# Kernel optimization log

Measured on AMD Instinct MI355X. Metric: run time of the kernel, lower is better.

## Reference

```python
import jax, jax.numpy as jnp
import numpy as np

NB_TS = 4          # module-level global nb_timestep in the original code
EMBED = 512
SQRT_DIM = float(np.sqrt(EMBED))


def _conv(x, w, b=None):
    # torch Conv2d(kernel=3, stride=1, padding=1), NCHW / OIHW
    y = jax.lax.conv_general_dilated(x, w, (1, 1), ((1, 1), (1, 1)),
                                     dimension_numbers=('NCHW', 'OIHW', 'NCHW'))
    if b is not None:
        y = y + b[None, :, None, None]
    return y


def setup_inputs() -> dict:
    B, C, H, W = 8, 512, 16, 16
    TXT = 256
    key = jax.random.key(0)
    ks = iter(jax.random.split(key, 40))

    def nrm(shape, s=0.02):
        return jax.random.normal(next(ks), shape, jnp.float32) * s

    inp = {
        'x':   jax.random.normal(next(ks), (B, C, H, W), jnp.float32),
        'txt': jax.random.normal(next(ks), (B, 1, TXT), jnp.float32),
        # attention convs
        'Wa_w': nrm((C, C, 3, 3)), 'Wa_b': nrm((C,)),
        'Ua_w': nrm((C, C, 3, 3)), 'Ua_b': nrm((C,)),
        'Va_w': nrm((1, C, 3, 3)),
        # gate convs
        'Wi_w': nrm((C, C, 3, 3)), 'Wi_b': nrm((C,)),
        'Ui_w': nrm((C, C, 3, 3)), 'Ui_b': nrm((C,)),
        'Wf_w': nrm((C, C, 3, 3)), 'Wf_b': nrm((C,)),
        'Uf_w': nrm((C, C, 3, 3)), 'Uf_b': nrm((C,)),
        'Wc_w': nrm((C, C, 3, 3)), 'Wc_b': nrm((C,)),
        'Uc_w': nrm((C, C, 3, 3)), 'Uc_b': nrm((C,)),
        'Wo_w': nrm((C, C, 3, 3)), 'Wo_b': nrm((C,)),
        'Uo_w': nrm((C, C, 3, 3)), 'Uo_b': nrm((C,)),
        # text attention linears (torch Linear weight layout [out, in])
        'WQ': nrm((EMBED * H * W, TXT)),
        'WK': nrm((EMBED, 1)),
        'WV': nrm((EMBED, 1)),
        'Wsum_w': nrm((1, EMBED)), 'Wsum_b': nrm((1,)),
    }
    return inp


def reference(x, txt, Wa_w, Wa_b, Ua_w, Ua_b, Va_w,
              Wi_w, Wi_b, Ui_w, Ui_b, Wf_w, Wf_b, Uf_w, Uf_b,
              Wc_w, Wc_b, Uc_w, Uc_b, Wo_w, Wo_b, Uo_w, Uo_b,
              WQ, WK, WV, Wsum_w, Wsum_b):
    B, _, Hs, Ws = x.shape
    txt2 = txt.reshape(txt.shape[0], txt.shape[2])  # [B, 256]
    h = x
    c = x
    # Q is timestep-invariant; hoist out of the loop (same math)
    Q = (txt2 @ WQ.T).reshape(B, Hs, Ws, EMBED)  # [B,H,W,E]
    for _ in range(NB_TS):
        Z = _conv(jnp.tanh(_conv(h, Wa_w, Wa_b) + _conv(x, Ua_w, Ua_b)), Va_w)  # [B,1,H,W]
        A1 = jax.nn.softmax(Z, axis=1)          # softmax over channel dim of size 1 (faithful)
        Ap = jnp.transpose(A1, (0, 2, 3, 1))    # [B,H,W,1]
        K = Ap @ WK.T                            # [B,H,W,E]
        V = Ap @ WV.T                            # [B,H,W,E]
        scores = jnp.sum(Q * K, axis=3, keepdims=True) / SQRT_DIM  # [B,H,W,1]
        attn = jax.nn.softmax(scores, axis=1)    # torch softmax(dim=1) -> over H axis
        # repeat(...,embed_dim)*V is just a broadcast multiply
        A2 = (attn * V) @ Wsum_w.T + Wsum_b      # [B,H,W,1]
        A2 = jnp.transpose(A2, (0, 3, 1, 2))     # [B,1,H,W]
        myA = A1 + A2
        AM = myA * x
        i = jax.nn.sigmoid(_conv(AM, Wi_w, Wi_b) + _conv(h, Ui_w, Ui_b))
        f = jax.nn.sigmoid(_conv(AM, Wf_w, Wf_b) + _conv(h, Uf_w, Uf_b))
        o = jax.nn.sigmoid(_conv(AM, Wo_w, Wo_b) + _conv(h, Uo_w, Uo_b))
        g = jnp.tanh(_conv(AM, Wc_w, Wc_b) + _conv(h, Uc_w, Uc_b))
        c = g * i + f * c
        h = jnp.tanh(c) * o
    return h
```

## Files before the change

### kernel.cpp

```cpp
#include <hip/hip_runtime.h>

typedef unsigned short u16;
typedef __attribute__((ext_vector_type(8))) _Float16 f16x8;
typedef __attribute__((ext_vector_type(4))) float f32x4;
typedef __attribute__((ext_vector_type(4))) int i32x4;
typedef __attribute__((ext_vector_type(4))) unsigned short us4;

__device__ __forceinline__ u16 f2h(float f) {
  _Float16 h = (_Float16)f;
  return __builtin_bit_cast(unsigned short, h);
}
__device__ __forceinline__ float sigm(float v) { return 1.0f / (1.0f + __expf(-v)); }
__device__ __forceinline__ float tanh_(float v) {
  float t = __expf(-2.0f * fabsf(v));
  float r = (1.0f - t) / (1.0f + t);
  return v >= 0.0f ? r : -r;
}

typedef const __attribute__((address_space(1))) unsigned int* gas_t;
typedef __attribute__((address_space(3))) unsigned int* las_t;
__device__ __forceinline__ void gl16(const u16* g, u16* l) {
  __builtin_amdgcn_global_load_lds((gas_t)g, (las_t)l, 16, 0, 0);
}

__global__ __launch_bounds__(256, 4) void prep_scores(
    const float* __restrict__ WQ, const float* __restrict__ WK,
    const float* __restrict__ txt, const float* __restrict__ WV,
    const float* __restrict__ Wsw, const float* __restrict__ Wsb,
    float* __restrict__ scores, float* __restrict__ sb) {
  __shared__ float red[4][8];
  __shared__ float red2[4];
  int tid = threadIdx.x;
  int p = blockIdx.x & 255;
  int es = blockIdx.x >> 8;
  int t4 = tid & 63, eg = tid >> 6;
  const f32x4* base = (const f32x4*)WQ + ((size_t)p * 512 + es * 64 + eg * 16) * 64 + t4;
  f32x4 va[16];
#pragma unroll
  for (int i = 0; i < 16; ++i) va[i] = base[i * 64];
  f32x4 wkq[4];
  const f32x4* wkp = (const f32x4*)(WK + es * 64 + eg * 16);
#pragma unroll
  for (int i = 0; i < 4; ++i) wkq[i] = wkp[i];
  __builtin_amdgcn_sched_barrier(0);
  f32x4 m4 = {0.f, 0.f, 0.f, 0.f};
#pragma unroll
  for (int i = 0; i < 4; ++i)
#pragma unroll
    for (int e = 0; e < 4; ++e) m4 += va[i * 4 + e] * wkq[i][e];
  float v[8];
  const f32x4* txp = (const f32x4*)txt;
#pragma unroll
  for (int b = 0; b < 8; ++b) {
    f32x4 tx = txp[b * 64 + t4];
    v[b] = m4[0] * tx[0] + m4[1] * tx[1] + m4[2] * tx[2] + m4[3] * tx[3];
  }
#pragma unroll
  for (int off = 32; off; off >>= 1)
#pragma unroll
    for (int b = 0; b < 8; ++b) v[b] += __shfl_down(v[b], off, 64);
  if (t4 == 0)
#pragma unroll
    for (int b = 0; b < 8; ++b) red[eg][b] = v[b];
  __syncthreads();
  if (tid < 8) {
    float sv = red[0][tid] + red[1][tid] + red[2][tid] + red[3][tid];
    atomicAdd(&scores[tid * 256 + p], sv * 0.044194173824159216f);
  }
  if (blockIdx.x == 0) {
    float vv = WV[tid] * Wsw[tid] + WV[tid + 256] * Wsw[tid + 256];
#pragma unroll
    for (int off = 32; off; off >>= 1) vv += __shfl_down(vv, off, 64);
    if (t4 == 0) red2[eg] = vv;
    __syncthreads();
    if (tid == 0) {
      sb[0] = red2[0] + red2[1] + red2[2] + red2[3];
      sb[1] = Wsb[0];
    }
  }
}

__global__ __launch_bounds__(256, 4) void prep_swz(
    const float* __restrict__ wi, const float* __restrict__ wf,
    const float* __restrict__ wo, const float* __restrict__ wc,
    const float* __restrict__ ui, const float* __restrict__ uf,
    const float* __restrict__ uo, const float* __restrict__ uc,
    u16* __restrict__ dstW, u16* __restrict__ dstU) {
  int tid = threadIdx.x;
  int sbid = blockIdx.x;
  int set = sbid >> 9;
  int chgrp = (sbid >> 4) & 31;
  int chunk = sbid & 15;
  int q = tid & 3, gch = tid >> 2;
  int gate = gch >> 4, chrow = gch & 15;
  int ch = chgrp * 16 + chrow;
  const float* s;
  if (set == 0) s = gate == 0 ? wi : gate == 1 ? wf : gate == 2 ? wo : wc;
  else          s = gate == 0 ? ui : gate == 1 ? uf : gate == 2 ? uo : uc;
  const f32x4* src = (const f32x4*)(s + (size_t)(ch * 512 + chunk * 32) * 9) + q * 18;
  f32x4 va[18];
#pragma unroll
  for (int i = 0; i < 18; ++i) va[i] = src[i];
  __builtin_amdgcn_sched_barrier(0);
  u16* dst = (set == 0 ? dstW : dstU) + (size_t)(chgrp * 16 + chunk) * 18432
             + (size_t)(gate * 64 + q * 16 + chrow) * 8;
#pragma unroll
  for (int k9 = 0; k9 < 9; ++k9) {
    i32x4 wv;
#pragma unroll
    for (int w = 0; w < 4; ++w) {
      int i0 = (2 * w) * 9 + k9, i1 = (2 * w + 1) * 9 + k9;
      unsigned lo = f2h(va[i0 >> 2][i0 & 3]);
      unsigned hi = f2h(va[i1 >> 2][i1 & 3]);
      wv[w] = (int)(lo | (hi << 16));
    }
    *(i32x4*)(dst + k9 * 2048) = wv;
  }
}

__global__ void prep_inputs(const float* __restrict__ x, const float* __restrict__ scores,
                            const float* __restrict__ sb,
                            u16* __restrict__ AM, u16* __restrict__ H0) {
  __shared__ float sc[16];
  int idx = blockIdx.x * 256 + threadIdx.x;
  int ch = idx & 511, p = (idx >> 9) & 255, b = idx >> 17;
  int w = p & 15, h = p >> 4;
  if (threadIdx.x < 16) sc[threadIdx.x] = scores[b * 256 + threadIdx.x * 16 + w];
  __syncthreads();
  float s = sb[0], b0 = sb[1];
  float mx = -1e30f;
#pragma unroll
  for (int hh = 0; hh < 16; ++hh) mx = fmaxf(mx, sc[hh]);
  float den = 0.f, my = 0.f;
#pragma unroll
  for (int hh = 0; hh < 16; ++hh) {
    float e = __expf(sc[hh] - mx);
    den += e;
    if (hh == h) my = e;
  }
  float coef = 1.0f + b0 + s * my / den;
  float xv = x[(size_t)(b * 512 + ch) * 256 + p];
  AM[idx] = f2h(coef * xv);
  H0[idx] = f2h(xv);
}

template <int MODE>
__launch_bounds__(512, 2)
__global__ void conv4(const u16* __restrict__ inA, const u16* __restrict__ inH,
                      const u16* __restrict__ wW, const u16* __restrict__ wU,
                      const float* __restrict__ bWi, const float* __restrict__ bUi,
                      const float* __restrict__ bWf, const float* __restrict__ bUf,
                      const float* __restrict__ bWo, const float* __restrict__ bUo,
                      const float* __restrict__ bWc, const float* __restrict__ bUc,
                      float* __restrict__ G, const float* __restrict__ c_src,
                      float* __restrict__ c_dst, u16* __restrict__ h_out,
                      float* __restrict__ out) {
  __shared__ __align__(16) u16 Alds[2][9 * 4 * 64 * 8];
  __shared__ __align__(16) u16 Blds[2][18 * 18 * 32];
  const int tid = threadIdx.x;
  const int chgrp = blockIdx.x & 31;
  const int b = blockIdx.x >> 5;
  const int wave = tid >> 6, lane = tid & 63;
  const int row = lane & 15, quad = lane >> 4;
  const int nw = wave & 3, mw = wave >> 2;
  const int NCH = (MODE == 0) ? 32 : 16;

  {
    i32x4 z = {0, 0, 0, 0};
    i32x4* bz = (i32x4*)&Blds[0][0];
#pragma unroll
    for (int i = 0; i < 6; ++i) {
      int k = tid + 512 * i;
      if (k < 2592) bz[k] = z;
    }
  }
  __syncthreads();

  const u16* wsrcW = wW + (size_t)chgrp * 294912;
  const u16* wsrcU = wU + (size_t)chgrp * 294912;
  const u16* isrcA = inA + (size_t)b * 131072;
  const u16* isrcH = inH + (size_t)b * 131072;

  auto stage = [&](int k, int bb) {
    const u16* gw;
    const u16* gi;
    if (MODE == 0 && k < 16) { gw = wsrcW + k * 18432; gi = isrcA + k * 32; }
    else                     { gw = wsrcU + (k & 15) * 18432; gi = isrcH + (k & 15) * 32; }
    u16* Ab = &Alds[bb][0];
#pragma unroll
    for (int i = 0; i < 5; ++i) {
      int idx = i * 8 + wave;
      if (idx < 36) gl16(gw + (idx * 64 + lane) * 8, &Ab[idx * 512]);
    }
    u16* Bb = &Blds[bb][0];
    int xi = lane >> 2;
    int qsrc = (lane & 3) ^ (((xi + 1) >> 2) & 3);
#pragma unroll
    for (int j = 0; j < 2; ++j) {
      int gy = wave + j * 8;
      gl16(gi + (size_t)(gy * 16 + xi) * 512 + qsrc * 8, &Bb[(gy + 1) * 576 + 32]);
    }
  };

  f32x4 acc[2][4];
#pragma unroll
  for (int m = 0; m < 2; ++m)
#pragma unroll
    for (int jj = 0; jj < 4; ++jj) acc[m][jj] = (f32x4){0.f, 0.f, 0.f, 0.f};

  const int ch0 = chgrp * 16 + quad * 4;
  float* gptr = G + (size_t)blockIdx.x * 16384 + wave * 2048 + lane * 4;

  stage(0, 0);
  __syncthreads();
  int bb = 0;

#pragma unroll 1
  for (int k = 0; k < NCH; ++k) {
    if (k + 1 < NCH) stage(k + 1, bb ^ 1);
    const u16* Ab = &Alds[bb][0];
    const u16* Bb = &Blds[bb][0];
#pragma unroll
    for (int kx = 0; kx < 3; ++kx) {
      int xx = row + kx;
      int qs = quad ^ ((xx >> 2) & 3);
      f16x8 bfr[6];
#pragma unroll
      for (int rr = 0; rr < 6; ++rr)
        bfr[rr] = *(const f16x8*)(&Bb[(4 * nw + rr) * 576 + xx * 32 + qs * 8]);
      f16x8 afr[6];
#pragma unroll
      for (int ky = 0; ky < 3; ++ky)
#pragma unroll
        for (int m = 0; m < 2; ++m)
          afr[ky * 2 + m] = *(const f16x8*)(&Ab[((ky * 3 + kx) * 4 + 2 * mw + m) * 512 + lane * 8]);
#pragma unroll
      for (int ky = 0; ky < 3; ++ky)
#pragma unroll
        for (int m = 0; m < 2; ++m)
#pragma unroll
          for (int jj = 0; jj < 4; ++jj)
            acc[m][jj] = __builtin_amdgcn_mfma_f32_16x16x32_f16(afr[ky * 2 + m], bfr[jj + ky],
                                                                acc[m][jj], 0, 0, 0);
    }
    if constexpr (MODE == 0) {
      if (k == 15) {
#pragma unroll
        for (int m = 0; m < 2; ++m) {
          int g = 2 * mw + m;
          const float* bw = g == 0 ? bWi : g == 1 ? bWf : g == 2 ? bWo : bWc;
          const float* bu = g == 0 ? bUi : g == 1 ? bUf : g == 2 ? bUo : bUc;
          f32x4 bias;
#pragma unroll
          for (int r = 0; r < 4; ++r) bias[r] = bw[ch0 + r] + bu[ch0 + r];
#pragma unroll
          for (int jj = 0; jj < 4; ++jj) {
            acc[m][jj] = acc[m][jj] + bias;
            *(f32x4*)(gptr + (m * 4 + jj) * 256) = acc[m][jj];
          }
        }
      }
    }
    __syncthreads();
    bb ^= 1;
  }

  if constexpr (MODE != 0) {
#pragma unroll
    for (int m = 0; m < 2; ++m)
#pragma unroll
      for (int jj = 0; jj < 4; ++jj)
        acc[m][jj] = acc[m][jj] + *(const f32x4*)(gptr + (m * 4 + jj) * 256);
  }
  float* X = (float*)&Blds[0][0];
  if (mw == 1) {
#pragma unroll
    for (int m = 0; m < 2; ++m)
#pragma unroll
      for (int jj = 0; jj < 4; ++jj)
        *(f32x4*)(X + (size_t)(((nw * 2 + m) * 4 + jj) * 256) + lane * 4) = acc[m][jj];
  }
  __syncthreads();
  if (mw == 0) {
#pragma unroll
    for (int jj = 0; jj < 4; ++jj) {
      const int p = (4 * nw + jj) * 16 + row;
      f32x4 zi = acc[0][jj], zf = acc[1][jj];
      f32x4 zo = *(const f32x4*)(X + (size_t)(((nw * 2 + 0) * 4 + jj) * 256) + lane * 4);
      f32x4 zg = *(const f32x4*)(X + (size_t)(((nw * 2 + 1) * 4 + jj) * 256) + lane * 4);
      f32x4 cold;
#pragma unroll
      for (int r = 0; r < 4; ++r)
        cold[r] = c_src[(size_t)(b * 512 + ch0 + r) * 256 + p];
      f32x4 cnew, hv;
#pragma unroll
      for (int r = 0; r < 4; ++r) {
        float iv = sigm(zi[r]);
        float fv = sigm(zf[r]);
        float ov = sigm(zo[r]);
        float gv = tanh_(zg[r]);
        float cn = fmaf(gv, iv, fv * cold[r]);
        cnew[r] = cn;
        hv[r] = tanh_(cn) * ov;
      }
      if constexpr (MODE != 2) {
#pragma unroll
        for (int r = 0; r < 4; ++r)
          c_dst[(size_t)(b * 512 + ch0 + r) * 256 + p] = cnew[r];
        us4 hb;
        hb[0] = f2h(hv[0]); hb[1] = f2h(hv[1]);
        hb[2] = f2h(hv[2]); hb[3] = f2h(hv[3]);
        *(us4*)(h_out + (size_t)b * 131072 + (size_t)p * 512 + ch0) = hb;
      } else {
#pragma unroll
        for (int r = 0; r < 4; ++r)
          out[(size_t)(b * 512 + ch0 + r) * 256 + p] = hv[r];
      }
    }
  }
}

extern "C" void kernel_launch(void* const* d_in, const int* in_sizes, int n_in,
                              void* d_out, int out_size, void* d_ws, size_t ws_size,
                              hipStream_t stream) {
  const float* x    = (const float*)d_in[0];
  const float* txt  = (const float*)d_in[1];
  const float* Wi_w = (const float*)d_in[7];
  const float* Wi_b = (const float*)d_in[8];
  const float* Ui_w = (const float*)d_in[9];
  const float* Ui_b = (const float*)d_in[10];
  const float* Wf_w = (const float*)d_in[11];
  const float* Wf_b = (const float*)d_in[12];
  const float* Uf_w = (const float*)d_in[13];
  const float* Uf_b = (const float*)d_in[14];
  const float* Wc_w = (const float*)d_in[15];
  const float* Wc_b = (const float*)d_in[16];
  const float* Uc_w = (const float*)d_in[17];
  const float* Uc_b = (const float*)d_in[18];
  const float* Wo_w = (const float*)d_in[19];
  const float* Wo_b = (const float*)d_in[20];
  const float* Uo_w = (const float*)d_in[21];
  const float* Uo_b = (const float*)d_in[22];
  const float* WQ   = (const float*)d_in[23];
  const float* WK   = (const float*)d_in[24];
  const float* WV   = (const float*)d_in[25];
  const float* Wsw  = (const float*)d_in[26];
  const float* Wsb  = (const float*)d_in[27];
  (void)in_sizes; (void)n_in; (void)ws_size;

  char* ws = (char*)d_ws;
  size_t off = 0;
  auto carve = [&](size_t n) {
    char* p = ws + off;
    off += (n + 255) & ~(size_t)255;
    return p;
  };
  u16* WswzW    = (u16*)carve(18874368);
  u16* WswzU    = (u16*)carve(18874368);
  u16* AM       = (u16*)carve(2097152);
  u16* H0       = (u16*)carve(2097152);
  u16* H1       = (u16*)carve(2097152);
  float* G      = (float*)carve(16777216);
  float* C      = (float*)carve(4194304);
  float* scores = (float*)carve(8192);
  float* sb     = (float*)carve(256);

  hipMemsetAsync(scores, 0, 8192, stream);

  prep_scores<<<2048, 256, 0, stream>>>(WQ, WK, txt, WV, Wsw, Wsb, scores, sb);
  prep_swz<<<1024, 256, 0, stream>>>(Wi_w, Wf_w, Wo_w, Wc_w,
                                     Ui_w, Uf_w, Uo_w, Uc_w, WswzW, WswzU);
  prep_inputs<<<4096, 256, 0, stream>>>(x, scores, sb, AM, H0);

  conv4<0><<<256, 512, 0, stream>>>(AM, H0, WswzW, WswzU,
                                    Wi_b, Ui_b, Wf_b, Uf_b, Wo_b, Uo_b, Wc_b, Uc_b,
                                    G, x, C, H1, nullptr);
  conv4<1><<<256, 512, 0, stream>>>(nullptr, H1, nullptr, WswzU,
                                    nullptr, nullptr, nullptr, nullptr,
                                    nullptr, nullptr, nullptr, nullptr,
                                    G, C, C, H0, nullptr);
  conv4<1><<<256, 512, 0, stream>>>(nullptr, H0, nullptr, WswzU,
                                    nullptr, nullptr, nullptr, nullptr,
                                    nullptr, nullptr, nullptr, nullptr,
                                    G, C, C, H1, nullptr);
  conv4<2><<<256, 512, 0, stream>>>(nullptr, H1, nullptr, WswzU,
                                    nullptr, nullptr, nullptr, nullptr,
                                    nullptr, nullptr, nullptr, nullptr,
                                    G, C, nullptr, nullptr, (float*)d_out);
}
```

Baseline: 508.2 us.

## Store activations pre-padded, split conv blocks by row half, restage prep loads

Activations AM/H0/H1 are now stored in a zero-padded 18x18 NHWC layout, so the conv kernel reads input fragments straight from global memory instead of staging the image tile through LDS. Each batch image is split across two blocks by row half, which doubles the grid and raises the occupancy target. The WQ score kernel now loads through LDS with global_load_lds, and the weight swizzle kernel uses 512 threads with smaller per-thread chunks. The cost is extra memsets for the padded buffers, and the conv B-operand reads now go uncached through global/L2 with redundant loads across waves, trading LDS traffic for more latency and memory traffic.

```diff
diff --git a/kernel.cpp b/kernel.cpp
--- a/kernel.cpp
+++ b/kernel.cpp
@@ -23,45 +23,45 @@
   __builtin_amdgcn_global_load_lds((gas_t)g, (las_t)l, 16, 0, 0);
 }
 
-__global__ __launch_bounds__(256, 4) void prep_scores(
+__global__ __launch_bounds__(256) void prep_scores(
     const float* __restrict__ WQ, const float* __restrict__ WK,
     const float* __restrict__ txt, const float* __restrict__ WV,
     const float* __restrict__ Wsw, const float* __restrict__ Wsb,
     float* __restrict__ scores, float* __restrict__ sb) {
+  __shared__ __align__(16) float L[64 * 256];
+  __shared__ float wk[64];
   __shared__ float red[4][8];
   __shared__ float red2[4];
   int tid = threadIdx.x;
+  int lane = tid & 63, wave = tid >> 6;
   int p = blockIdx.x & 255;
   int es = blockIdx.x >> 8;
-  int t4 = tid & 63, eg = tid >> 6;
-  const f32x4* base = (const f32x4*)WQ + ((size_t)p * 512 + es * 64 + eg * 16) * 64 + t4;
-  f32x4 va[16];
-#pragma unroll
-  for (int i = 0; i < 16; ++i) va[i] = base[i * 64];
-  f32x4 wkq[4];
-  const f32x4* wkp = (const f32x4*)(WK + es * 64 + eg * 16);
-#pragma unroll
-  for (int i = 0; i < 4; ++i) wkq[i] = wkp[i];
-  __builtin_amdgcn_sched_barrier(0);
-  f32x4 m4 = {0.f, 0.f, 0.f, 0.f};
-#pragma unroll
-  for (int i = 0; i < 4; ++i)
-#pragma unroll
-    for (int e = 0; e < 4; ++e) m4 += va[i * 4 + e] * wkq[i][e];
+  const float* src = WQ + ((size_t)p * 512 + es * 64 + wave * 16) * 256;
+  u16* ldst = (u16*)&L[wave * 16 * 256];
+#pragma unroll
+  for (int r = 0; r < 16; ++r)
+    gl16((const u16*)(src + (size_t)r * 256 + lane * 4), ldst + r * 512);
+  if (tid < 64) wk[tid] = WK[es * 64 + tid];
+  __syncthreads();
+  float a0 = 0.f, a1 = 0.f, a2 = 0.f, a3 = 0.f;
+#pragma unroll
+  for (int e = 0; e < 64; e += 4) {
+    a0 = fmaf(L[(e + 0) * 256 + tid], wk[e + 0], a0);
+    a1 = fmaf(L[(e + 1) * 256 + tid], wk[e + 1], a1);
+    a2 = fmaf(L[(e + 2) * 256 + tid], wk[e + 2], a2);
+    a3 = fmaf(L[(e + 3) * 256 + tid], wk[e + 3], a3);
+  }
+  float m = (a0 + a1) + (a2 + a3);
   float v[8];
-  const f32x4* txp = (const f32x4*)txt;
-#pragma unroll
-  for (int b = 0; b < 8; ++b) {
-    f32x4 tx = txp[b * 64 + t4];
-    v[b] = m4[0] * tx[0] + m4[1] * tx[1] + m4[2] * tx[2] + m4[3] * tx[3];
-  }
+#pragma unroll
+  for (int b = 0; b < 8; ++b) v[b] = m * txt[b * 256 + tid];
 #pragma unroll
   for (int off = 32; off; off >>= 1)
 #pragma unroll
     for (int b = 0; b < 8; ++b) v[b] += __shfl_down(v[b], off, 64);
-  if (t4 == 0)
-#pragma unroll
-    for (int b = 0; b < 8; ++b) red[eg][b] = v[b];
+  if (lane == 0)
+#pragma unroll
+    for (int b = 0; b < 8; ++b) red[wave][b] = v[b];
   __syncthreads();
   if (tid < 8) {
     float sv = red[0][tid] + red[1][tid] + red[2][tid] + red[3][tid];
@@ -71,7 +71,7 @@
     float vv = WV[tid] * Wsw[tid] + WV[tid + 256] * Wsw[tid + 256];
 #pragma unroll
     for (int off = 32; off; off >>= 1) vv += __shfl_down(vv, off, 64);
-    if (t4 == 0) red2[eg] = vv;
+    if (lane == 0) red2[wave] = vv;
     __syncthreads();
     if (tid == 0) {
       sb[0] = red2[0] + red2[1] + red2[2] + red2[3];
@@ -80,41 +80,37 @@
   }
 }
 
-__global__ __launch_bounds__(256, 4) void prep_swz(
+__global__ __launch_bounds__(512) void prep_swz(
     const float* __restrict__ wi, const float* __restrict__ wf,
     const float* __restrict__ wo, const float* __restrict__ wc,
     const float* __restrict__ ui, const float* __restrict__ uf,
     const float* __restrict__ uo, const float* __restrict__ uc,
     u16* __restrict__ dstW, u16* __restrict__ dstU) {
   int tid = threadIdx.x;
-  int sbid = blockIdx.x;
-  int set = sbid >> 9;
-  int chgrp = (sbid >> 4) & 31;
-  int chunk = sbid & 15;
-  int q = tid & 3, gch = tid >> 2;
-  int gate = gch >> 4, chrow = gch & 15;
+  int set = blockIdx.x >> 9;
+  int chgrp = (blockIdx.x >> 4) & 31;
+  int chunk = blockIdx.x & 15;
+  int gate = tid >> 7, chrow = (tid >> 3) & 15, oct = tid & 7;
+  int q = oct >> 1, c0 = (oct & 1) * 4;
   int ch = chgrp * 16 + chrow;
   const float* s;
   if (set == 0) s = gate == 0 ? wi : gate == 1 ? wf : gate == 2 ? wo : wc;
   else          s = gate == 0 ? ui : gate == 1 ? uf : gate == 2 ? uo : uc;
-  const f32x4* src = (const f32x4*)(s + (size_t)(ch * 512 + chunk * 32) * 9) + q * 18;
-  f32x4 va[18];
-#pragma unroll
-  for (int i = 0; i < 18; ++i) va[i] = src[i];
-  __builtin_amdgcn_sched_barrier(0);
+  const f32x4* src = (const f32x4*)(s + ((size_t)(ch * 512 + chunk * 32) + q * 8 + c0) * 9);
+  f32x4 va[9];
+#pragma unroll
+  for (int i = 0; i < 9; ++i) va[i] = src[i];
   u16* dst = (set == 0 ? dstW : dstU) + (size_t)(chgrp * 16 + chunk) * 18432
-             + (size_t)(gate * 64 + q * 16 + chrow) * 8;
+             + (size_t)(gate * 64 + q * 16 + chrow) * 8 + c0;
 #pragma unroll
   for (int k9 = 0; k9 < 9; ++k9) {
-    i32x4 wv;
-#pragma unroll
-    for (int w = 0; w < 4; ++w) {
-      int i0 = (2 * w) * 9 + k9, i1 = (2 * w + 1) * 9 + k9;
-      unsigned lo = f2h(va[i0 >> 2][i0 & 3]);
-      unsigned hi = f2h(va[i1 >> 2][i1 & 3]);
-      wv[w] = (int)(lo | (hi << 16));
-    }
-    *(i32x4*)(dst + k9 * 2048) = wv;
+    us4 wv;
+#pragma unroll
+    for (int c = 0; c < 4; ++c) {
+      int i = c * 9 + k9;
+      wv[c] = f2h(va[i >> 2][i & 3]);
+    }
+    *(us4*)(dst + (size_t)k9 * 2048) = wv;
   }
 }
 
@@ -140,12 +136,13 @@
   }
   float coef = 1.0f + b0 + s * my / den;
   float xv = x[(size_t)(b * 512 + ch) * 256 + p];
-  AM[idx] = f2h(coef * xv);
-  H0[idx] = f2h(xv);
+  size_t o = (size_t)b * 165888 + (size_t)((h + 1) * 18 + (w + 1)) * 512 + ch;
+  AM[o] = f2h(coef * xv);
+  H0[o] = f2h(xv);
 }
 
 template <int MODE>
-__launch_bounds__(512, 2)
+__launch_bounds__(512, 4)
 __global__ void conv4(const u16* __restrict__ inA, const u16* __restrict__ inH,
                       const u16* __restrict__ wW, const u16* __restrict__ wU,
                       const float* __restrict__ bWi, const float* __restrict__ bUi,
@@ -156,93 +153,74 @@
                       float* __restrict__ c_dst, u16* __restrict__ h_out,
                       float* __restrict__ out) {
   __shared__ __align__(16) u16 Alds[2][9 * 4 * 64 * 8];
-  __shared__ __align__(16) u16 Blds[2][18 * 18 * 32];
   const int tid = threadIdx.x;
   const int chgrp = blockIdx.x & 31;
-  const int b = blockIdx.x >> 5;
+  const int nhalf = (blockIdx.x >> 5) & 1;
+  const int b = blockIdx.x >> 6;
   const int wave = tid >> 6, lane = tid & 63;
   const int row = lane & 15, quad = lane >> 4;
   const int nw = wave & 3, mw = wave >> 2;
   const int NCH = (MODE == 0) ? 32 : 16;
-
-  {
-    i32x4 z = {0, 0, 0, 0};
-    i32x4* bz = (i32x4*)&Blds[0][0];
-#pragma unroll
-    for (int i = 0; i < 6; ++i) {
-      int k = tid + 512 * i;
-      if (k < 2592) bz[k] = z;
-    }
-  }
-  __syncthreads();
+  const int r0 = nhalf * 8 + nw * 2;
 
   const u16* wsrcW = wW + (size_t)chgrp * 294912;
   const u16* wsrcU = wU + (size_t)chgrp * 294912;
-  const u16* isrcA = inA + (size_t)b * 131072;
-  const u16* isrcH = inH + (size_t)b * 131072;
-
-  auto stage = [&](int k, int bb) {
-    const u16* gw;
-    const u16* gi;
-    if (MODE == 0 && k < 16) { gw = wsrcW + k * 18432; gi = isrcA + k * 32; }
-    else                     { gw = wsrcU + (k & 15) * 18432; gi = isrcH + (k & 15) * 32; }
+  const u16* imgA = inA + (size_t)b * 165888;
+  const u16* imgH = inH + (size_t)b * 165888;
+
+  auto stageA = [&](int k, int bb) {
+    const u16* gw = (MODE == 0 && k < 16) ? wsrcW + k * 18432 : wsrcU + (k & 15) * 18432;
     u16* Ab = &Alds[bb][0];
 #pragma unroll
     for (int i = 0; i < 5; ++i) {
       int idx = i * 8 + wave;
       if (idx < 36) gl16(gw + (idx * 64 + lane) * 8, &Ab[idx * 512]);
     }
-    u16* Bb = &Blds[bb][0];
-    int xi = lane >> 2;
-    int qsrc = (lane & 3) ^ (((xi + 1) >> 2) & 3);
-#pragma unroll
-    for (int j = 0; j < 2; ++j) {
-      int gy = wave + j * 8;
-      gl16(gi + (size_t)(gy * 16 + xi) * 512 + qsrc * 8, &Bb[(gy + 1) * 576 + 32]);
-    }
   };
 
-  f32x4 acc[2][4];
+  f32x4 acc[2][2];
 #pragma unroll
   for (int m = 0; m < 2; ++m)
 #pragma unroll
-    for (int jj = 0; jj < 4; ++jj) acc[m][jj] = (f32x4){0.f, 0.f, 0.f, 0.f};
+    for (int n = 0; n < 2; ++n) acc[m][n] = (f32x4){0.f, 0.f, 0.f, 0.f};
 
   const int ch0 = chgrp * 16 + quad * 4;
-  float* gptr = G + (size_t)blockIdx.x * 16384 + wave * 2048 + lane * 4;
-
-  stage(0, 0);
+  float* gptr = G + (size_t)blockIdx.x * 8192 + wave * 1024 + lane * 4;
+
+  stageA(0, 0);
   __syncthreads();
   int bb = 0;
 
 #pragma unroll 1
   for (int k = 0; k < NCH; ++k) {
-    if (k + 1 < NCH) stage(k + 1, bb ^ 1);
+    if (k + 1 < NCH) stageA(k + 1, bb ^ 1);
+    const u16* img = (MODE == 0 && k < 16) ? imgA : imgH;
+    const u16* ibase = img + (size_t)(k & 15) * 32 + quad * 8;
+    f16x8 bfr[3][4];
+#pragma unroll
+    for (int kx = 0; kx < 3; ++kx)
+#pragma unroll
+      for (int jj = 0; jj < 4; ++jj)
+        bfr[kx][jj] = *(const f16x8*)(ibase + (size_t)((r0 + jj) * 18 + row + kx) * 512);
     const u16* Ab = &Alds[bb][0];
-    const u16* Bb = &Blds[bb][0];
 #pragma unroll
     for (int kx = 0; kx < 3; ++kx) {
-      int xx = row + kx;
-      int qs = quad ^ ((xx >> 2) & 3);
-      f16x8 bfr[6];
-#pragma unroll
-      for (int rr = 0; rr < 6; ++rr)
-        bfr[rr] = *(const f16x8*)(&Bb[(4 * nw + rr) * 576 + xx * 32 + qs * 8]);
       f16x8 afr[6];
 #pragma unroll
       for (int ky = 0; ky < 3; ++ky)
 #pragma unroll
         for (int m = 0; m < 2; ++m)
-          afr[ky * 2 + m] = *(const f16x8*)(&Ab[((ky * 3 + kx) * 4 + 2 * mw + m) * 512 + lane * 8]);
+          afr[ky * 2 + m] = *(const f16x8*)(&Alds[bb][((ky * 3 + kx) * 4 + 2 * mw + m) * 512 + lane * 8]);
 #pragma unroll
       for (int ky = 0; ky < 3; ++ky)
 #pragma unroll
         for (int m = 0; m < 2; ++m)
 #pragma unroll
-          for (int jj = 0; jj < 4; ++jj)
-            acc[m][jj] = __builtin_amdgcn_mfma_f32_16x16x32_f16(afr[ky * 2 + m], bfr[jj + ky],
-                                                                acc[m][jj], 0, 0, 0);
-    }
+          for (int n = 0; n < 2; ++n)
+            acc[m][n] = __builtin_amdgcn_mfma_f32_16x16x32_f16(afr[ky * 2 + m], bfr[kx][n + ky],
+                                                               acc[m][n], 0, 0, 0);
+    }
+    (void)Ab;
     if constexpr (MODE == 0) {
       if (k == 15) {
 #pragma unroll
@@ -254,9 +232,9 @@
 #pragma unroll
           for (int r = 0; r < 4; ++r) bias[r] = bw[ch0 + r] + bu[ch0 + r];
 #pragma unroll
-          for (int jj = 0; jj < 4; ++jj) {
-            acc[m][jj] = acc[m][jj] + bias;
-            *(f32x4*)(gptr + (m * 4 + jj) * 256) = acc[m][jj];
+          for (int n = 0; n < 2; ++n) {
+            acc[m][n] = acc[m][n] + bias;
+            *(f32x4*)(gptr + (m * 2 + n) * 256) = acc[m][n];
           }
         }
       }
@@ -269,25 +247,25 @@
 #pragma unroll
     for (int m = 0; m < 2; ++m)
 #pragma unroll
-      for (int jj = 0; jj < 4; ++jj)
-        acc[m][jj] = acc[m][jj] + *(const f32x4*)(gptr + (m * 4 + jj) * 256);
-  }
-  float* X = (float*)&Blds[0][0];
+      for (int n = 0; n < 2; ++n)
+        acc[m][n] = acc[m][n] + *(const f32x4*)(gptr + (m * 2 + n) * 256);
+  }
+  float* X = (float*)&Alds[0][0];
   if (mw == 1) {
 #pragma unroll
     for (int m = 0; m < 2; ++m)
 #pragma unroll
-      for (int jj = 0; jj < 4; ++jj)
-        *(f32x4*)(X + (size_t)(((nw * 2 + m) * 4 + jj) * 256) + lane * 4) = acc[m][jj];
+      for (int n = 0; n < 2; ++n)
+        *(f32x4*)(X + (size_t)((nw * 4 + m * 2 + n) * 256) + lane * 4) = acc[m][n];
   }
   __syncthreads();
   if (mw == 0) {
 #pragma unroll
-    for (int jj = 0; jj < 4; ++jj) {
-      const int p = (4 * nw + jj) * 16 + row;
-      f32x4 zi = acc[0][jj], zf = acc[1][jj];
-      f32x4 zo = *(const f32x4*)(X + (size_t)(((nw * 2 + 0) * 4 + jj) * 256) + lane * 4);
-      f32x4 zg = *(const f32x4*)(X + (size_t)(((nw * 2 + 1) * 4 + jj) * 256) + lane * 4);
+    for (int n = 0; n < 2; ++n) {
+      const int p = (r0 + n) * 16 + row;
+      f32x4 zi = acc[0][n], zf = acc[1][n];
+      f32x4 zo = *(const f32x4*)(X + (size_t)((nw * 4 + n) * 256) + lane * 4);
+      f32x4 zg = *(const f32x4*)(X + (size_t)((nw * 4 + 2 + n) * 256) + lane * 4);
       f32x4 cold;
 #pragma unroll
       for (int r = 0; r < 4; ++r)
@@ -310,7 +288,7 @@
         us4 hb;
         hb[0] = f2h(hv[0]); hb[1] = f2h(hv[1]);
         hb[2] = f2h(hv[2]); hb[3] = f2h(hv[3]);
-        *(us4*)(h_out + (size_t)b * 131072 + (size_t)p * 512 + ch0) = hb;
+        *(us4*)(h_out + (size_t)b * 165888 + (size_t)((r0 + n + 1) * 18 + row + 1) * 512 + ch0) = hb;
       } else {
 #pragma unroll
         for (int r = 0; r < 4; ++r)
@@ -357,33 +335,36 @@
   };
   u16* WswzW    = (u16*)carve(18874368);
   u16* WswzU    = (u16*)carve(18874368);
-  u16* AM       = (u16*)carve(2097152);
-  u16* H0       = (u16*)carve(2097152);
-  u16* H1       = (u16*)carve(2097152);
+  u16* AM       = (u16*)carve(2654208);
+  u16* H0       = (u16*)carve(2654208);
+  u16* H1       = (u16*)carve(2654208);
   float* G      = (float*)carve(16777216);
   float* C      = (float*)carve(4194304);
   float* scores = (float*)carve(8192);
   float* sb     = (float*)carve(256);
 
   hipMemsetAsync(scores, 0, 8192, stream);
+  hipMemsetAsync(AM, 0, 2654208, stream);
+  hipMemsetAsync(H0, 0, 2654208, stream);
+  hipMemsetAsync(H1, 0, 2654208, stream);
 
   prep_scores<<<2048, 256, 0, stream>>>(WQ, WK, txt, WV, Wsw, Wsb, scores, sb);
-  prep_swz<<<1024, 256, 0, stream>>>(Wi_w, Wf_w, Wo_w, Wc_w,
+  prep_swz<<<1024, 512, 0, stream>>>(Wi_w, Wf_w, Wo_w, Wc_w,
                                      Ui_w, Uf_w, Uo_w, Uc_w, WswzW, WswzU);
   prep_inputs<<<4096, 256, 0, stream>>>(x, scores, sb, AM, H0);
 
-  conv4<0><<<256, 512, 0, stream>>>(AM, H0, WswzW, WswzU,
+  conv4<0><<<512, 512, 0, stream>>>(AM, H0, WswzW, WswzU,
                                     Wi_b, Ui_b, Wf_b, Uf_b, Wo_b, Uo_b, Wc_b, Uc_b,
                                     G, x, C, H1, nullptr);
-  conv4<1><<<256, 512, 0, stream>>>(nullptr, H1, nullptr, WswzU,
+  conv4<1><<<512, 512, 0, stream>>>(nullptr, H1, nullptr, WswzU,
                                     nullptr, nullptr, nullptr, nullptr,
                                     nullptr, nullptr, nullptr, nullptr,
                                     G, C, C, H0, nullptr);
-  conv4<1><<<256, 512, 0, stream>>>(nullptr, H0, nullptr, WswzU,
+  conv4<1><<<512, 512, 0, stream>>>(nullptr, H0, nullptr, WswzU,
                                     nullptr, nullptr, nullptr, nullptr,
                                     nullptr, nullptr, nullptr, nullptr,
                                     G, C, C, H1, nullptr);
-  conv4<2><<<256, 512, 0, stream>>>(nullptr, H1, nullptr, WswzU,
+  conv4<2><<<512, 512, 0, stream>>>(nullptr, H1, nullptr, WswzU,
                                     nullptr, nullptr, nullptr, nullptr,
                                     nullptr, nullptr, nullptr, nullptr,
                                     G, C, nullptr, nullptr, (float*)d_out);
```

New measurement: 809.6 us. 1.59x slower.
